# Kernel optimization log

Hardware: AMD Instinct MI355X
Metric: run time of the kernel (lower is better)

## Reference

```python
import jax, jax.numpy as jnp
import numpy as np

KERNEL = 8


def setup_inputs() -> dict:
    key = jax.random.key(0)
    ks = jax.random.split(key, 9)
    N, Cin, L = 16, 128, 2048
    Cout = 256
    x = jax.random.normal(ks[0], (N, Cin, L), dtype=jnp.float32)
    conv_w = jax.random.normal(ks[1], (Cout, Cin, KERNEL), dtype=jnp.float32) * (1.0 / np.sqrt(Cin * KERNEL))
    conv_b = jax.random.normal(ks[2], (Cout,), dtype=jnp.float32) * 0.01
    wq = jax.random.normal(ks[3], (Cout, Cout), dtype=jnp.float32) * (1.0 / np.sqrt(Cout))
    bq = jax.random.normal(ks[4], (Cout,), dtype=jnp.float32) * 0.01
    wk = jax.random.normal(ks[5], (Cout, Cout), dtype=jnp.float32) * (1.0 / np.sqrt(Cout))
    bk = jax.random.normal(ks[6], (Cout,), dtype=jnp.float32) * 0.01
    wv = jax.random.normal(ks[7], (Cout, Cout), dtype=jnp.float32) * (1.0 / np.sqrt(Cout))
    bv = jax.random.normal(ks[8], (Cout,), dtype=jnp.float32) * 0.01
    return {"x": x, "conv_w": conv_w, "conv_b": conv_b,
            "wq": wq, "bq": bq, "wk": wk, "bk": bk, "wv": wv, "bv": bv}


def reference(x, conv_w, conv_b, wq, bq, wk, bk, wv, bv):
    # Conv1d, valid padding: [N, Cin, L] -> [N, Cout, S], S = L - KERNEL + 1
    h = jax.lax.conv_general_dilated(
        x, conv_w, window_strides=(1,), padding='VALID',
        dimension_numbers=('NCH', 'OIH', 'NCH'))
    h = jax.nn.relu(h + conv_b[None, :, None])
    N, C, S = h.shape
    h = jnp.transpose(h, (0, 2, 1))  # [N, S, C]
    # Linear layers (torch convention: y = x @ W^T + b)
    q = jnp.einsum('nsc,dc->nsd', h, wq) + bq
    k = jnp.einsum('nsc,dc->nsd', h, wk) + bk
    v = jnp.einsum('nsc,dc->nsd', h, wv) + bv
    # sigmoid (non-normalized) attention over full SxS scores
    scores = jnp.einsum('nsd,ntd->nst', q, k) / jnp.sqrt(jnp.asarray(C, h.dtype))
    attn = jax.nn.sigmoid(scores)  # [N, S, S]
    out = jnp.einsum('nst,ntd->nsd', attn, v)
    return jnp.transpose(out, (0, 2, 1))  # [N, C, S]
```

## Files before the change

### kernel.cpp

```cpp
#include <hip/hip_runtime.h>

typedef short short8 __attribute__((ext_vector_type(8)));
typedef float f32x4 __attribute__((ext_vector_type(4)));
typedef float f32x16 __attribute__((ext_vector_type(16)));
typedef unsigned short u16x4 __attribute__((ext_vector_type(4)));

constexpr int NB = 16, CIN = 128, LIN = 2048, CO = 256;
constexpr int SL = 2041;
constexpr int MT = NB * SL;
constexpr int MP = 32768;
constexpr int XTS = 136;

constexpr size_t XT_OFF = 0;
constexpr size_t XT_SZ  = (size_t)NB*LIN*XTS*2 + 65536;
constexpr size_t CW_OFF = XT_OFF + XT_SZ;
constexpr size_t CW_SZ  = (size_t)CO*CIN*8*2;
constexpr size_t WQ_OFF = CW_OFF + CW_SZ;
constexpr size_t WB_SZ  = (size_t)CO*CO*2;
constexpr size_t WK_OFF = WQ_OFF + WB_SZ;
constexpr size_t WV_OFF = WK_OFF + WB_SZ;
constexpr size_t H_OFF  = WV_OFF + WB_SZ;
constexpr size_t HB_SZ  = (size_t)MP*CO*2;
constexpr size_t Q_OFF  = H_OFF + HB_SZ;
constexpr size_t K_OFF  = Q_OFF + HB_SZ;
constexpr size_t VT_OFF = K_OFF + HB_SZ;

__device__ inline unsigned short f2bf(float f) {
  union { float f; unsigned int u; } v; v.f = f;
  unsigned int r = v.u + 0x7fffu + ((v.u >> 16) & 1u);
  return (unsigned short)(r >> 16);
}

__device__ inline void sync_lds() {
  __asm__ volatile("" ::: "memory");
  __builtin_amdgcn_s_waitcnt(0xc07f);
  __builtin_amdgcn_s_barrier();
  __asm__ volatile("" ::: "memory");
}
__device__ inline void barrier_only() {
  __asm__ volatile("" ::: "memory");
  __builtin_amdgcn_s_barrier();
  __asm__ volatile("" ::: "memory");
}

#if defined(__has_builtin)
#if __has_builtin(__builtin_amdgcn_global_load_lds)
#define HAVE_GLDS 1
#endif
#endif

__device__ inline void gld16(const unsigned short* g, void* l) {
#ifdef HAVE_GLDS
  __builtin_amdgcn_global_load_lds(
      (const __attribute__((address_space(1))) void*)g,
      (__attribute__((address_space(3))) void*)l, 16, 0, 0);
#else
  *(short8*)l = *(const short8*)g;
#endif
}

__global__ __launch_bounds__(256) void prep_kernel(
    const float* __restrict__ x, unsigned short* __restrict__ xt,
    const float* __restrict__ cw_in, unsigned short* __restrict__ cw_out,
    const float* __restrict__ wq, const float* __restrict__ wk, const float* __restrict__ wv,
    unsigned short* __restrict__ wqb, unsigned short* __restrict__ wkb,
    unsigned short* __restrict__ wvb) {
  __shared__ float tile[32][33];
  const int b = blockIdx.x;
  const int tid = threadIdx.x;
  if (b < 4096) {
    const int tx = tid & 31, ty = tid >> 5;
    const int s0 = (b & 63) * 32, c0 = ((b >> 6) & 3) * 32, n = b >> 8;
    #pragma unroll
    for (int r = 0; r < 4; ++r)
      tile[ty * 4 + r][tx] = x[((size_t)(n * CIN + c0 + ty * 4 + r)) * LIN + s0 + tx];
    __syncthreads();
    #pragma unroll
    for (int r = 0; r < 4; ++r)
      xt[((size_t)(n * LIN + s0 + ty * 4 + r)) * XTS + c0 + tx] = f2bf(tile[tx][ty * 4 + r]);
  } else if (b < 4096 + 1024) {
    int idx = (b - 4096) * 256 + tid;
    int co = idx >> 10, r = idx & 1023, kp = r >> 7, ci = r & 127;
    cw_out[idx] = f2bf(cw_in[co * 1024 + ci * 8 + kp]);
  } else {
    int lb2 = b - (4096 + 1024);
    int z = lb2 >> 6, lb = lb2 & 63;
    const float* src = (z == 0) ? wq : (z == 1) ? wk : wv;
    unsigned short* dst = (z == 0) ? wqb : (z == 1) ? wkb : wvb;
    int i = (lb * 256 + tid) * 4;
    float4 v = *(const float4*)(src + i);
    u16x4 r;
    r.x = f2bf(v.x); r.y = f2bf(v.y); r.z = f2bf(v.z); r.w = f2bf(v.w);
    *(u16x4*)(dst + i) = r;
  }
}

__global__ __launch_bounds__(256) void conv_gemm(
    const unsigned short* __restrict__ xt,
    const unsigned short* __restrict__ wb,
    const float* __restrict__ bias,
    unsigned short* __restrict__ h)
{
  __shared__ unsigned short sX[18432];
  __shared__ unsigned short sB[2][4096];
  const int tid = threadIdx.x;
  const int w = tid >> 6, lane = tid & 63, quad = lane >> 4, l16 = lane & 15;
  const int n  = blockIdx.y;
  const int s0 = blockIdx.x * 128;
  const int d0 = blockIdx.z * 128;

  {
    const unsigned short* xbase = xt + ((size_t)n * LIN + s0) * XTS;
    #pragma unroll
    for (int i = 0; i < 9; ++i) {
      int u = i * 256 + tid;
      gld16(xbase + u * 8, ((char*)sX) + u * 16);
    }
  }

  const int brow0 = tid >> 2, bkgs = tid & 3;
  short8 breg[2];
  #pragma unroll
  for (int i2 = 0; i2 < 2; ++i2) {
    int row = i2 * 64 + brow0;
    int kg = bkgs ^ ((row >> 1) & 3);
    breg[i2] = *(const short8*)(wb + (size_t)(d0 + row) * 1024 + kg * 8);
  }
  #pragma unroll
  for (int i2 = 0; i2 < 2; ++i2)
    *(short8*)(&sB[0][(i2 * 256 + tid) * 8]) = breg[i2];
  __syncthreads();

  f32x4 acc[2][8];
  #pragma unroll
  for (int i = 0; i < 2; ++i)
    #pragma unroll
    for (int j = 0; j < 8; ++j) acc[i][j] = (f32x4){0.f, 0.f, 0.f, 0.f};

  for (int kc = 0; kc < 32; ++kc) {
    const int kcn = (kc < 31) ? kc + 1 : kc;
    const int kpn = kcn >> 2, ci0n = (kcn & 3) * 32;
    #pragma unroll
    for (int i2 = 0; i2 < 2; ++i2) {
      int row = i2 * 64 + brow0;
      int kg = bkgs ^ ((row >> 1) & 3);
      breg[i2] = *(const short8*)(wb + (size_t)(d0 + row) * 1024 + kpn * 128 + ci0n + kg * 8);
    }

    const int kp = kc >> 2, ci0 = (kc & 3) * 32;
    const unsigned short* sBc = sB[kc & 1];
    short8 bfr[8];
    #pragma unroll
    for (int j = 0; j < 8; ++j) {
      int r = j * 16 + l16;
      bfr[j] = *(const short8*)(sBc + r * 32 + (quad ^ ((r >> 1) & 3)) * 8);
    }
    #pragma unroll
    for (int i = 0; i < 2; ++i) {
      int srow = w * 32 + i * 16 + l16;
      short8 afr = *(const short8*)(sX + (srow + kp) * XTS + ci0 + quad * 8);
      #pragma unroll
      for (int j = 0; j < 8; ++j)
        acc[i][j] = __builtin_amdgcn_mfma_f32_16x16x32_bf16(afr, bfr[j], acc[i][j], 0, 0, 0);
    }

    #pragma unroll
    for (int i2 = 0; i2 < 2; ++i2)
      *(short8*)(&sB[(kc + 1) & 1][(i2 * 256 + tid) * 8]) = breg[i2];
    sync_lds();
  }

  #pragma unroll
  for (int i = 0; i < 2; ++i)
    #pragma unroll
    for (int j = 0; j < 8; ++j) {
      int col = d0 + j * 16 + l16;
      float bv = bias[col];
      #pragma unroll
      for (int jj = 0; jj < 4; ++jj) {
        int s = s0 + w * 32 + i * 16 + quad * 4 + jj;
        if (s < SL) {
          float val = fmaxf(acc[i][j][jj] + bv, 0.f);
          h[(size_t)(n * SL + s) * CO + col] = f2bf(val);
        }
      }
    }
}

__global__ __launch_bounds__(256) void lin_gemm(
    const unsigned short* __restrict__ A,
    const unsigned short* __restrict__ Bq, const unsigned short* __restrict__ Bk,
    const unsigned short* __restrict__ Bv,
    const float* __restrict__ biq, const float* __restrict__ bik,
    const float* __restrict__ biv,
    unsigned short* __restrict__ qb, unsigned short* __restrict__ kb,
    unsigned short* __restrict__ vtb)
{
  __shared__ unsigned short sA[2][4096];
  __shared__ unsigned short sB[2][4096];
  const int tid = threadIdx.x;
  const int w = tid >> 6, lane = tid & 63, quad = lane >> 4, l16 = lane & 15;
  const int m0 = blockIdx.x * 128, d0 = blockIdx.y * 128, z = blockIdx.z;
  const unsigned short* B = (z == 0) ? Bq : (z == 1) ? Bk : Bv;
  const float* bias        = (z == 0) ? biq : (z == 1) ? bik : biv;

  const int brow0 = tid >> 2, bkgs = tid & 3;
  short8 areg[2], breg[2];
  #pragma unroll
  for (int i2 = 0; i2 < 2; ++i2) {
    int row = i2 * 64 + brow0;
    int kg = bkgs ^ ((row >> 1) & 3);
    areg[i2] = *(const short8*)(A + (size_t)(m0 + row) * CO + kg * 8);
    breg[i2] = *(const short8*)(B + (size_t)(d0 + row) * CO + kg * 8);
  }
  #pragma unroll
  for (int i2 = 0; i2 < 2; ++i2) {
    *(short8*)(&sA[0][(i2 * 256 + tid) * 8]) = areg[i2];
    *(short8*)(&sB[0][(i2 * 256 + tid) * 8]) = breg[i2];
  }
  sync_lds();

  f32x4 acc[2][8];
  #pragma unroll
  for (int i = 0; i < 2; ++i)
    #pragma unroll
    for (int j = 0; j < 8; ++j) acc[i][j] = (f32x4){0.f, 0.f, 0.f, 0.f};

  for (int kc = 0; kc < 8; ++kc) {
    const int kcn = (kc < 7) ? kc + 1 : kc;
    #pragma unroll
    for (int i2 = 0; i2 < 2; ++i2) {
      int row = i2 * 64 + brow0;
      int kg = bkgs ^ ((row >> 1) & 3);
      areg[i2] = *(const short8*)(A + (size_t)(m0 + row) * CO + kcn * 32 + kg * 8);
      breg[i2] = *(const short8*)(B + (size_t)(d0 + row) * CO + kcn * 32 + kg * 8);
    }

    const unsigned short* sAc = sA[kc & 1];
    const unsigned short* sBc = sB[kc & 1];
    short8 afr[2], bfr[8];
    #pragma unroll
    for (int i = 0; i < 2; ++i) {
      int r = w * 32 + i * 16 + l16;
      afr[i] = *(const short8*)(sAc + r * 32 + (quad ^ ((r >> 1) & 3)) * 8);
    }
    #pragma unroll
    for (int j = 0; j < 8; ++j) {
      int r = j * 16 + l16;
      bfr[j] = *(const short8*)(sBc + r * 32 + (quad ^ ((r >> 1) & 3)) * 8);
    }
    #pragma unroll
    for (int i = 0; i < 2; ++i)
      #pragma unroll
      for (int j = 0; j < 8; ++j)
        acc[i][j] = __builtin_amdgcn_mfma_f32_16x16x32_bf16(afr[i], bfr[j], acc[i][j], 0, 0, 0);

    #pragma unroll
    for (int i2 = 0; i2 < 2; ++i2) {
      *(short8*)(&sA[(kc + 1) & 1][(i2 * 256 + tid) * 8]) = areg[i2];
      *(short8*)(&sB[(kc + 1) & 1][(i2 * 256 + tid) * 8]) = breg[i2];
    }
    sync_lds();
  }

  #pragma unroll
  for (int i = 0; i < 2; ++i)
    #pragma unroll
    for (int j = 0; j < 8; ++j) {
      int col = d0 + j * 16 + l16;
      float bv = bias[col];
      #pragma unroll
      for (int jj = 0; jj < 4; ++jj) {
        int m = m0 + w * 32 + i * 16 + quad * 4 + jj;
        float val = acc[i][j][jj] + bv;
        if (z < 2) {
          ((z == 0) ? qb : kb)[(size_t)m * CO + col] = f2bf(val);
        } else if (m < MT) {
          int nn = m / SL, ss = m - nn * SL;
          vtb[(size_t)col * MP + nn * 2048 + ss] = f2bf(val);
        }
      }
    }
}

__global__ __launch_bounds__(512, 2) void attn_kernel(
    const unsigned short* __restrict__ qb,
    const unsigned short* __restrict__ kb,
    const unsigned short* __restrict__ vtb,
    float* __restrict__ out)
{
  __shared__ unsigned short sK[2][16384];
  __shared__ unsigned short sV[2][16384];
  __shared__ unsigned short sP[8192];
  const int tid = threadIdx.x;
  const int w = tid >> 6, lane = tid & 63;
  const int half = lane >> 5, l32 = lane & 31;
  const int bidx = blockIdx.x;
  const int n = (bidx & 7) + ((bidx >> 7) << 3);
  const int s0 = ((bidx >> 3) & 15) * 128;
  const int sr = w & 3, tr = w >> 2;

  const unsigned short* kbN = kb + (size_t)(n * SL) * CO;
  const unsigned short* vbN = vtb + (size_t)n * 2048;

#define STAGE_TILE(buf, tk)                                                      \
  {                                                                              \
    _Pragma("unroll")                                                            \
    for (int i = 0; i < 4; ++i) {                                                \
      int u = i * 512 + tid;                                                     \
      int t = u >> 5, sl = u & 31;                                               \
      gld16(kbN + (size_t)((tk) + t) * CO + ((sl ^ (t & 31)) << 3),              \
            ((char*)sK[buf]) + u * 16);                                          \
    }                                                                            \
    _Pragma("unroll")                                                            \
    for (int i = 0; i < 4; ++i) {                                                \
      int u = i * 512 + tid;                                                     \
      int d = u >> 3, sl = u & 7;                                                \
      gld16(vbN + (size_t)d * MP + (tk) + ((sl ^ (d & 7)) << 3),                 \
            ((char*)sV[buf]) + u * 16);                                          \
    }                                                                            \
  }

  STAGE_TILE(0, 0)

  short8 qf[16];
  {
    const unsigned short* qp = qb + (size_t)(n * SL + s0 + sr * 32 + l32) * CO + half * 8;
    #pragma unroll
    for (int kk = 0; kk < 16; ++kk) qf[kk] = *(const short8*)(qp + kk * 16);
  }

  __builtin_amdgcn_s_waitcnt(0x0F70);
  barrier_only();

  f32x16 o[4];
  #pragma unroll
  for (int di = 0; di < 4; ++di)
    #pragma unroll
    for (int r = 0; r < 16; ++r) o[di][r] = 0.f;

  for (int it = 0; it < 32; ++it) {
    const int cur = it & 1;
    if (it < 31) {
      STAGE_TILE(cur ^ 1, (it + 1) * 64)
      __builtin_amdgcn_s_waitcnt(0x0F78);
    } else {
      __builtin_amdgcn_s_waitcnt(0x0F70);
    }
    barrier_only();

    const unsigned short* sKc = sK[cur];
    const int tl = tr * 32 + l32;
    f32x16 sacc;
    #pragma unroll
    for (int r = 0; r < 16; ++r) sacc[r] = 0.f;
    #pragma unroll
    for (int kk = 0; kk < 16; ++kk) {
      short8 kf = *(const short8*)(sKc + tl * 256 + (((kk * 2 + half) ^ (tl & 31)) << 3));
      sacc = __builtin_amdgcn_mfma_f32_32x32x16_bf16(kf, qf[kk], sacc, 0, 0, 0);
    }

    const int t0 = it * 64;
    #pragma unroll
    for (int q2 = 0; q2 < 4; ++q2) {
      u16x4 pk;
      #pragma unroll
      for (int e = 0; e < 4; ++e) {
        int tg = t0 + tr * 32 + 8 * q2 + 4 * half + e;
        float p = __builtin_amdgcn_rcpf(1.f + __expf(-sacc[q2 * 4 + e] * 0.0625f));
        pk[e] = (tg < SL) ? f2bf(p) : (unsigned short)0;
      }
      *(u16x4*)(sP + ((tr * 4 + q2) * 128 + sr * 32 + l32) * 8 + 4 * half) = pk;
    }
    sync_lds();

    const unsigned short* sVc = sV[cur];
    #pragma unroll
    for (int kt = 0; kt < 4; ++kt) {
      int g = kt * 2 + half;
      short8 pa = *(const short8*)(sP + ((g << 7) + sr * 32 + l32) * 8);
      #pragma unroll
      for (int di = 0; di < 4; ++di) {
        int d = tr * 128 + di * 32 + l32;
        short8 vf = *(const short8*)(sVc + d * 64 + ((g ^ (d & 7)) << 3));
        o[di] = __builtin_amdgcn_mfma_f32_32x32x16_bf16(vf, pa, o[di], 0, 0, 0);
      }
    }
    sync_lds();
  }

  const int s = s0 + sr * 32 + l32;
  if (s < SL) {
    float* op = out + (size_t)n * CO * SL + s;
    #pragma unroll
    for (int di = 0; di < 4; ++di)
      #pragma unroll
      for (int r = 0; r < 16; ++r) {
        int d = tr * 128 + di * 32 + (r & 3) + 8 * (r >> 2) + 4 * half;
        __builtin_nontemporal_store(o[di][r], op + (size_t)d * SL);
      }
  }
#undef STAGE_TILE
}

extern "C" void kernel_launch(void* const* d_in, const int* in_sizes, int n_in,
                              void* d_out, int out_size, void* d_ws, size_t ws_size,
                              hipStream_t stream) {
  const float* x      = (const float*)d_in[0];
  const float* conv_w = (const float*)d_in[1];
  const float* conv_b = (const float*)d_in[2];
  const float* wq     = (const float*)d_in[3];
  const float* bq     = (const float*)d_in[4];
  const float* wk     = (const float*)d_in[5];
  const float* bk     = (const float*)d_in[6];
  const float* wv     = (const float*)d_in[7];
  const float* bv     = (const float*)d_in[8];

  char* ws = (char*)d_ws;
  unsigned short* xt  = (unsigned short*)(ws + XT_OFF);
  unsigned short* cw  = (unsigned short*)(ws + CW_OFF);
  unsigned short* wqb = (unsigned short*)(ws + WQ_OFF);
  unsigned short* wkb = (unsigned short*)(ws + WK_OFF);
  unsigned short* wvb = (unsigned short*)(ws + WV_OFF);
  unsigned short* hb  = (unsigned short*)(ws + H_OFF);
  unsigned short* qb  = (unsigned short*)(ws + Q_OFF);
  unsigned short* kb  = (unsigned short*)(ws + K_OFF);
  unsigned short* vtb = (unsigned short*)(ws + VT_OFF);

  hipLaunchKernelGGL(prep_kernel, dim3(4096 + 1024 + 192), dim3(256), 0, stream,
                     x, xt, conv_w, cw, wq, wk, wv, wqb, wkb, wvb);
  hipLaunchKernelGGL(conv_gemm, dim3(16, 16, 2), dim3(256), 0, stream, xt, cw, conv_b, hb);
  hipLaunchKernelGGL(lin_gemm,  dim3(256, 2, 3), dim3(256), 0, stream,
                     hb, wqb, wkb, wvb, bq, bk, bv, qb, kb, vtb);
  hipLaunchKernelGGL(attn_kernel, dim3(256), dim3(512), 0, stream,
                     qb, kb, vtb, (float*)d_out);
}
```

Baseline: 240.2 us.

## Software-pipeline attention loop so QK of next tile overlaps PV of previous

Restructures the attention main loop so each iteration computes QK^T and the sigmoid for tile `it` while running the PV MFMAs for tile `it-1`. The probability buffer becomes double-buffered, and K and V staging are split so V is fetched one iteration later. This leaves one barrier per iteration instead of two and adds s_setprio around the MFMA bursts, aiming to keep the matrix units busy across the sigmoid and LDS-write phases. In exchange, LDS use grows to the full 160KB, and there is one extra drain iteration.

```diff
diff --git a/kernel.cpp b/kernel.cpp
--- a/kernel.cpp
+++ b/kernel.cpp
@@ -291,7 +291,7 @@
 {
   __shared__ unsigned short sK[2][16384];
   __shared__ unsigned short sV[2][16384];
-  __shared__ unsigned short sP[8192];
+  __shared__ unsigned short sP[2][8192];
   const int tid = threadIdx.x;
   const int w = tid >> 6, lane = tid & 63;
   const int half = lane >> 5, l32 = lane & 31;
@@ -303,7 +303,7 @@
   const unsigned short* kbN = kb + (size_t)(n * SL) * CO;
   const unsigned short* vbN = vtb + (size_t)n * 2048;
 
-#define STAGE_TILE(buf, tk)                                                      \
+#define STAGE_K(buf, tk)                                                         \
   {                                                                              \
     _Pragma("unroll")                                                            \
     for (int i = 0; i < 4; ++i) {                                                \
@@ -312,6 +312,9 @@
       gld16(kbN + (size_t)((tk) + t) * CO + ((sl ^ (t & 31)) << 3),              \
             ((char*)sK[buf]) + u * 16);                                          \
     }                                                                            \
+  }
+#define STAGE_V(buf, tk)                                                         \
+  {                                                                              \
     _Pragma("unroll")                                                            \
     for (int i = 0; i < 4; ++i) {                                                \
       int u = i * 512 + tid;                                                     \
@@ -321,7 +324,7 @@
     }                                                                            \
   }
 
-  STAGE_TILE(0, 0)
+  STAGE_K(0, 0)
 
   short8 qf[16];
   {
@@ -339,54 +342,63 @@
     #pragma unroll
     for (int r = 0; r < 16; ++r) o[di][r] = 0.f;
 
-  for (int it = 0; it < 32; ++it) {
+  for (int it = 0; it <= 32; ++it) {
     const int cur = it & 1;
-    if (it < 31) {
-      STAGE_TILE(cur ^ 1, (it + 1) * 64)
-      __builtin_amdgcn_s_waitcnt(0x0F78);
-    } else {
+    if (it < 31) STAGE_K(cur ^ 1, (it + 1) * 64)
+    if (it < 32) STAGE_V(cur, it * 64)
+
+    f32x16 sacc;
+    if (it < 32) {
+      const unsigned short* sKc = sK[cur];
+      const int tl = tr * 32 + l32;
+      #pragma unroll
+      for (int r = 0; r < 16; ++r) sacc[r] = 0.f;
+      __builtin_amdgcn_s_setprio(1);
+      #pragma unroll
+      for (int kk = 0; kk < 16; ++kk) {
+        short8 kf = *(const short8*)(sKc + tl * 256 + (((kk * 2 + half) ^ (tl & 31)) << 3));
+        sacc = __builtin_amdgcn_mfma_f32_32x32x16_bf16(kf, qf[kk], sacc, 0, 0, 0);
+      }
+      __builtin_amdgcn_s_setprio(0);
+    }
+
+    if (it >= 1) {
+      const unsigned short* sVp = sV[cur ^ 1];
+      const unsigned short* sPp = sP[cur ^ 1];
+      __builtin_amdgcn_s_setprio(1);
+      #pragma unroll
+      for (int kt = 0; kt < 4; ++kt) {
+        int g = kt * 2 + half;
+        short8 pa = *(const short8*)(sPp + ((g << 7) + sr * 32 + l32) * 8);
+        #pragma unroll
+        for (int di = 0; di < 4; ++di) {
+          int d = tr * 128 + di * 32 + l32;
+          short8 vf = *(const short8*)(sVp + d * 64 + ((g ^ (d & 7)) << 3));
+          o[di] = __builtin_amdgcn_mfma_f32_32x32x16_bf16(vf, pa, o[di], 0, 0, 0);
+        }
+      }
+      __builtin_amdgcn_s_setprio(0);
+    }
+
+    if (it < 32) {
+      const int t0 = it * 64;
+      #pragma unroll
+      for (int q2 = 0; q2 < 4; ++q2) {
+        u16x4 pk;
+        #pragma unroll
+        for (int e = 0; e < 4; ++e) {
+          int tg = t0 + tr * 32 + 8 * q2 + 4 * half + e;
+          float p = __builtin_amdgcn_rcpf(1.f + __expf(-sacc[q2 * 4 + e] * 0.0625f));
+          pk[e] = (tg < SL) ? f2bf(p) : (unsigned short)0;
+        }
+        *(u16x4*)(sP[cur] + ((tr * 4 + q2) * 128 + sr * 32 + l32) * 8 + 4 * half) = pk;
+      }
+    }
+
+    if (it < 32) {
       __builtin_amdgcn_s_waitcnt(0x0F70);
-    }
-    barrier_only();
-
-    const unsigned short* sKc = sK[cur];
-    const int tl = tr * 32 + l32;
-    f32x16 sacc;
-    #pragma unroll
-    for (int r = 0; r < 16; ++r) sacc[r] = 0.f;
-    #pragma unroll
-    for (int kk = 0; kk < 16; ++kk) {
-      short8 kf = *(const short8*)(sKc + tl * 256 + (((kk * 2 + half) ^ (tl & 31)) << 3));
-      sacc = __builtin_amdgcn_mfma_f32_32x32x16_bf16(kf, qf[kk], sacc, 0, 0, 0);
-    }
-
-    const int t0 = it * 64;
-    #pragma unroll
-    for (int q2 = 0; q2 < 4; ++q2) {
-      u16x4 pk;
-      #pragma unroll
-      for (int e = 0; e < 4; ++e) {
-        int tg = t0 + tr * 32 + 8 * q2 + 4 * half + e;
-        float p = __builtin_amdgcn_rcpf(1.f + __expf(-sacc[q2 * 4 + e] * 0.0625f));
-        pk[e] = (tg < SL) ? f2bf(p) : (unsigned short)0;
-      }
-      *(u16x4*)(sP + ((tr * 4 + q2) * 128 + sr * 32 + l32) * 8 + 4 * half) = pk;
-    }
-    sync_lds();
-
-    const unsigned short* sVc = sV[cur];
-    #pragma unroll
-    for (int kt = 0; kt < 4; ++kt) {
-      int g = kt * 2 + half;
-      short8 pa = *(const short8*)(sP + ((g << 7) + sr * 32 + l32) * 8);
-      #pragma unroll
-      for (int di = 0; di < 4; ++di) {
-        int d = tr * 128 + di * 32 + l32;
-        short8 vf = *(const short8*)(sVc + d * 64 + ((g ^ (d & 7)) << 3));
-        o[di] = __builtin_amdgcn_mfma_f32_32x32x16_bf16(vf, pa, o[di], 0, 0, 0);
-      }
-    }
-    sync_lds();
+      sync_lds();
+    }
   }
 
   const int s = s0 + sr * 32 + l32;
@@ -400,7 +412,8 @@
         __builtin_nontemporal_store(o[di][r], op + (size_t)d * SL);
       }
   }
-#undef STAGE_TILE
+#undef STAGE_K
+#undef STAGE_V
 }
 
 extern "C" void kernel_launch(void* const* d_in, const int* in_sizes, int n_in,
```

Result: slower. 255.2 us (+6.2%).

## Pad sequence rows to 2048 and stage the V-transpose epilogue through LDS

Applied to the files above, without the earlier changes.

The h, q and k buffers now use a per-batch row stride of 2048 instead of 2041, so a 128-row GEMM tile never spans two batches and the row-index division disappears. The V projection epilogue first writes its bf16 tile into a swizzled shared-memory buffer, then emits coalesced 16-byte stores into the transposed V layout. Padded positions past the sequence end are zeroed. This replaces scattered 2-byte strided global writes. Padded h/q/k rows are no longer written, so correctness relies on V padding being zero and on the attention kernel tolerating whatever values sit in the unused K rows.

```diff
diff --git a/kernel.cpp b/kernel.cpp
--- a/kernel.cpp
+++ b/kernel.cpp
@@ -7,9 +7,9 @@
 
 constexpr int NB = 16, CIN = 128, LIN = 2048, CO = 256;
 constexpr int SL = 2041;
-constexpr int MT = NB * SL;
 constexpr int MP = 32768;
 constexpr int XTS = 136;
+
 
 constexpr size_t XT_OFF = 0;
 constexpr size_t XT_SZ  = (size_t)NB*LIN*XTS*2 + 65536;
@@ -181,7 +181,7 @@
         int s = s0 + w * 32 + i * 16 + quad * 4 + jj;
         if (s < SL) {
           float val = fmaxf(acc[i][j][jj] + bv, 0.f);
-          h[(size_t)(n * SL + s) * CO + col] = f2bf(val);
+          h[(size_t)(n * 2048 + s) * CO + col] = f2bf(val);
         }
       }
     }
@@ -196,8 +196,9 @@
     unsigned short* __restrict__ qb, unsigned short* __restrict__ kb,
     unsigned short* __restrict__ vtb)
 {
-  __shared__ unsigned short sA[2][4096];
-  __shared__ unsigned short sB[2][4096];
+  __shared__ unsigned short smem[16384];
+  unsigned short* const sAb = smem;
+  unsigned short* const sBb = smem + 8192;
   const int tid = threadIdx.x;
   const int w = tid >> 6, lane = tid & 63, quad = lane >> 4, l16 = lane & 15;
   const int m0 = blockIdx.x * 128, d0 = blockIdx.y * 128, z = blockIdx.z;
@@ -215,8 +216,8 @@
   }
   #pragma unroll
   for (int i2 = 0; i2 < 2; ++i2) {
-    *(short8*)(&sA[0][(i2 * 256 + tid) * 8]) = areg[i2];
-    *(short8*)(&sB[0][(i2 * 256 + tid) * 8]) = breg[i2];
+    *(short8*)(sAb + (i2 * 256 + tid) * 8) = areg[i2];
+    *(short8*)(sBb + (i2 * 256 + tid) * 8) = breg[i2];
   }
   sync_lds();
 
@@ -236,8 +237,8 @@
       breg[i2] = *(const short8*)(B + (size_t)(d0 + row) * CO + kcn * 32 + kg * 8);
     }
 
-    const unsigned short* sAc = sA[kc & 1];
-    const unsigned short* sBc = sB[kc & 1];
+    const unsigned short* sAc = sAb + (kc & 1) * 4096;
+    const unsigned short* sBc = sBb + (kc & 1) * 4096;
     short8 afr[2], bfr[8];
     #pragma unroll
     for (int i = 0; i < 2; ++i) {
@@ -257,30 +258,56 @@
 
     #pragma unroll
     for (int i2 = 0; i2 < 2; ++i2) {
-      *(short8*)(&sA[(kc + 1) & 1][(i2 * 256 + tid) * 8]) = areg[i2];
-      *(short8*)(&sB[(kc + 1) & 1][(i2 * 256 + tid) * 8]) = breg[i2];
+      *(short8*)(sAb + ((kc + 1) & 1) * 4096 + (i2 * 256 + tid) * 8) = areg[i2];
+      *(short8*)(sBb + ((kc + 1) & 1) * 4096 + (i2 * 256 + tid) * 8) = breg[i2];
     }
     sync_lds();
   }
 
-  #pragma unroll
-  for (int i = 0; i < 2; ++i)
-    #pragma unroll
-    for (int j = 0; j < 8; ++j) {
-      int col = d0 + j * 16 + l16;
-      float bv = bias[col];
-      #pragma unroll
-      for (int jj = 0; jj < 4; ++jj) {
-        int m = m0 + w * 32 + i * 16 + quad * 4 + jj;
-        float val = acc[i][j][jj] + bv;
-        if (z < 2) {
+  if (z < 2) {
+    #pragma unroll
+    for (int i = 0; i < 2; ++i)
+      #pragma unroll
+      for (int j = 0; j < 8; ++j) {
+        int col = d0 + j * 16 + l16;
+        float bv = bias[col];
+        #pragma unroll
+        for (int jj = 0; jj < 4; ++jj) {
+          int m = m0 + w * 32 + i * 16 + quad * 4 + jj;
+          float val = acc[i][j][jj] + bv;
           ((z == 0) ? qb : kb)[(size_t)m * CO + col] = f2bf(val);
-        } else if (m < MT) {
-          int nn = m / SL, ss = m - nn * SL;
-          vtb[(size_t)col * MP + nn * 2048 + ss] = f2bf(val);
         }
       }
-    }
+  } else {
+    #pragma unroll
+    for (int i = 0; i < 2; ++i)
+      #pragma unroll
+      for (int j = 0; j < 8; ++j) {
+        int c = j * 16 + l16;
+        float bv = bias[d0 + c];
+        int mb = w * 32 + i * 16 + quad * 4;
+        u16x4 pk;
+        #pragma unroll
+        for (int jj = 0; jj < 4; ++jj) pk[jj] = f2bf(acc[i][j][jj] + bv);
+        *(u16x4*)(smem + c * 128 + (mb ^ ((c & 7) << 3))) = pk;
+      }
+    sync_lds();
+    const int c = tid >> 1, mh = (tid & 1) * 64;
+    const int nn = m0 >> 11;
+    const int sbase = (m0 & 2047) + mh;
+    unsigned short* vrow = vtb + (size_t)(d0 + c) * MP + nn * 2048;
+    #pragma unroll
+    for (int b = 0; b < 8; ++b) {
+      int ss = sbase + b * 8;
+      short8 val = *(const short8*)(smem + c * 128 + ((mh + b * 8) ^ ((c & 7) << 3)));
+      if (ss + 7 >= SL) {
+        #pragma unroll
+        for (int e = 0; e < 8; ++e)
+          if (ss + e >= SL) val[e] = 0;
+      }
+      *(short8*)(vrow + ss) = val;
+    }
+  }
 }
 
 __global__ __launch_bounds__(512, 2) void attn_kernel(
@@ -300,7 +327,7 @@
   const int s0 = ((bidx >> 3) & 15) * 128;
   const int sr = w & 3, tr = w >> 2;
 
-  const unsigned short* kbN = kb + (size_t)(n * SL) * CO;
+  const unsigned short* kbN = kb + (size_t)(n * 2048) * CO;
   const unsigned short* vbN = vtb + (size_t)n * 2048;
 
 #define STAGE_TILE(buf, tk)                                                      \
@@ -325,7 +352,7 @@
 
   short8 qf[16];
   {
-    const unsigned short* qp = qb + (size_t)(n * SL + s0 + sr * 32 + l32) * CO + half * 8;
+    const unsigned short* qp = qb + (size_t)(n * 2048 + s0 + sr * 32 + l32) * CO + half * 8;
     #pragma unroll
     for (int kk = 0; kk < 16; ++kk) qf[kk] = *(const short8*)(qp + kk * 16);
   }
```

Measured after the change: 233.5 us. 1.03x faster.
